# Kernel tuning notes

Hardware: AMD Instinct MI355X
Metric: run time of the kernel (lower is better)

Reference implementation:

```python
import jax, jax.numpy as jnp
import numpy as np
import math

HIDDEN_DIM = 256
H2 = HIDDEN_DIM // 2  # 128
FEATURE_TEMPERATURE = math.sqrt(float(HIDDEN_DIM))


def setup_inputs() -> dict:
    key = jax.random.key(0)
    kf, ks, kw1, kb1, kw2, kb2 = jax.random.split(key, 6)
    B, N, D = 2, 1024, 256
    functional_hidden = jax.random.normal(kf, (B, N, D), dtype=jnp.float32)
    structural_hidden = jax.random.normal(ks, (B, N, D), dtype=jnp.float32)
    # relation_mlp params: Linear(1, H2) then Linear(H2, 1)
    bound1 = 1.0  # fan_in = 1
    w1 = jax.random.uniform(kw1, (H2,), jnp.float32, -bound1, bound1)
    b1 = jax.random.uniform(kb1, (H2,), jnp.float32, -bound1, bound1)
    bound2 = 1.0 / math.sqrt(H2)
    w2 = jax.random.uniform(kw2, (H2,), jnp.float32, -bound2, bound2)
    b2 = jax.random.uniform(kb2, (1,), jnp.float32, -bound2, bound2)
    return {"functional_hidden": functional_hidden, "structural_hidden": structural_hidden,
            "w1": w1, "b1": b1, "w2": w2, "b2": b2}


def reference(functional_hidden, structural_hidden, w1, b1, w2, b2):
    # center along feature dim
    fc = functional_hidden - jnp.mean(functional_hidden, axis=-1, keepdims=True)   # [B,N,D]
    sc = structural_hidden - jnp.mean(structural_hidden, axis=-1, keepdims=True)   # [B,N,D]
    # covariance: [B,N,N]
    covariance = jnp.einsum('bnd,bmd->bnm', fc, sc) / FEATURE_TEMPERATURE
    # per-row std norms (un-normalized, as in source: sqrt of sum of squares)
    f_std = jnp.maximum(jnp.sqrt(jnp.sum(fc * fc, axis=-1)), 1e-6)  # [B,N]
    s_std = jnp.maximum(jnp.sqrt(jnp.sum(sc * sc, axis=-1)), 1e-6)  # [B,N]
    denominator = jnp.maximum(f_std[:, :, None] * s_std[:, None, :], 1e-6)  # [B,N,N]
    correlation = jnp.clip(covariance / denominator, -1.0, 1.0)
    assortativity = jnp.exp(correlation)  # [B,N,N]
    # broadcast 2-layer MLP over every pair: Linear(1,H2)-GELU(exact)-Linear(H2,1)
    h = jax.nn.gelu(assortativity[..., None] * w1 + b1, approximate=False)  # [B,N,N,H2]
    out = jnp.einsum('bnmh,h->bnm', h, w2) + b2[0]  # [B,N,N]
    return out
```

## Files before the change

### kernel.cpp

```cpp
#include <hip/hip_runtime.h>
#include <math.h>

#define NB   2
#define NSEQ 1024
#define DD   256
#define LUTN 2048

#define BM 128
#define BN 64
#define MAGIC 0x5CA1AB1Eu

typedef _Float16 f16;
typedef _Float16 f16x8 __attribute__((ext_vector_type(8)));
typedef float f32x4 __attribute__((ext_vector_type(4)));

__device__ __forceinline__ float wrsum(float v) {
#pragma unroll
  for (int off = 32; off > 0; off >>= 1) v += __shfl_xor(v, off, 64);
  return v;
}

__global__ __launch_bounds__(512, 2) void fused_kernel(
    const float* __restrict__ fg, const float* __restrict__ sg,
    const float* __restrict__ w1, const float* __restrict__ b1,
    const float* __restrict__ w2, const float* __restrict__ b2,
    float* __restrict__ lut, unsigned* __restrict__ flags,
    float* __restrict__ out) {
  __shared__ __align__(16) f16 As[2][BM * 64];
  __shared__ __align__(16) f16 Bs[2][BN * 64];
  __shared__ float lut_s[LUTN + 1];
  __shared__ float mA[BM], rA[BM], mB[BN], rB[BN];

  const int t = threadIdx.x;
  const int lane = t & 63;
  const int w = t >> 6;
  const int wr = w >> 1, wc = w & 1;
  const int la = lane & 15;
  const int kg = lane >> 4;

  const int bid = blockIdx.x;
  const int x = bid & 7, k = bid >> 3;
  const int panel = x + 8 * (k >> 4);
  const int bz  = panel >> 3;
  const int bm0 = (panel & 7) * BM;
  const int bn0 = (k & 15) * BN;

  const float* fb = fg + ((size_t)bz * NSEQ + bm0) * DD;
  const float* sb = sg + ((size_t)bz * NSEQ + bn0) * DD;

  const int sr = t >> 2;
  const int so = t & 3;
  const bool doB = (t < 256);

  float4 A0[2], B0[2], A1[2], B1[2];
  float sAa = 0.f, qAa = 0.f, sBa = 0.f, qBa = 0.f;

  auto ld = [&](float4 (&a)[2], float4 (&b)[2], int st) {
    const float* p = &fb[(size_t)sr * DD + st * 32 + so * 8];
    a[0] = *reinterpret_cast<const float4*>(p);
    a[1] = *reinterpret_cast<const float4*>(p + 4);
    if (doB) {
      const float* q = &sb[(size_t)sr * DD + st * 32 + so * 8];
      b[0] = *reinterpret_cast<const float4*>(q);
      b[1] = *reinterpret_cast<const float4*>(q + 4);
    }
  };

  auto split8 = [](const float4& u0, const float4& u1, f16x8& hv, f16x8& lv,
                   float& sm, float& sq) {
    const float vals[8] = {u0.x, u0.y, u0.z, u0.w, u1.x, u1.y, u1.z, u1.w};
#pragma unroll
    for (int e = 0; e < 8; ++e) {
      sm += vals[e];
      sq = fmaf(vals[e], vals[e], sq);
      const f16 h = (f16)vals[e];
      hv[e] = h;
      lv[e] = (f16)(vals[e] - (float)h);
    }
  };

  auto cvt_write = [&](float4 (&a)[2], float4 (&b)[2], int pbuf) {
    f16x8 hv, lv;
    split8(a[0], a[1], hv, lv, sAa, qAa);
    *reinterpret_cast<f16x8*>(&As[pbuf][sr * 64 + ((so ^ (sr & 7)) << 3)]) = hv;
    *reinterpret_cast<f16x8*>(&As[pbuf][sr * 64 + (((4 + so) ^ (sr & 7)) << 3)]) = lv;
    if (doB) {
      split8(b[0], b[1], hv, lv, sBa, qBa);
      *reinterpret_cast<f16x8*>(&Bs[pbuf][sr * 64 + ((so ^ (sr & 7)) << 3)]) = hv;
      *reinterpret_cast<f16x8*>(&Bs[pbuf][sr * 64 + (((4 + so) ^ (sr & 7)) << 3)]) = lv;
    }
  };

  f32x4 acc[2][2] = {};

  auto do_mfma = [&](int p) {
    f16x8 ah[2], al[2], bh[2], bl[2];
#pragma unroll
    for (int i = 0; i < 2; ++i) {
      const int r = wr * 32 + 16 * i + la;
      ah[i] = *reinterpret_cast<const f16x8*>(&As[p][r * 64 + ((kg ^ (r & 7)) << 3)]);
      al[i] = *reinterpret_cast<const f16x8*>(&As[p][r * 64 + (((4 + kg) ^ (r & 7)) << 3)]);
    }
#pragma unroll
    for (int j = 0; j < 2; ++j) {
      const int r = wc * 32 + 16 * j + la;
      bh[j] = *reinterpret_cast<const f16x8*>(&Bs[p][r * 64 + ((kg ^ (r & 7)) << 3)]);
      bl[j] = *reinterpret_cast<const f16x8*>(&Bs[p][r * 64 + (((4 + kg) ^ (r & 7)) << 3)]);
    }
#pragma unroll
    for (int i = 0; i < 2; ++i)
#pragma unroll
      for (int j = 0; j < 2; ++j) {
        acc[i][j] = __builtin_amdgcn_mfma_f32_16x16x32_f16(ah[i], bh[j], acc[i][j], 0, 0, 0);
        acc[i][j] = __builtin_amdgcn_mfma_f32_16x16x32_f16(ah[i], bl[j], acc[i][j], 0, 0, 0);
        acc[i][j] = __builtin_amdgcn_mfma_f32_16x16x32_f16(al[i], bh[j], acc[i][j], 0, 0, 0);
      }
  };

  ld(A0, B0, 0);

  {
    const float w1a = w1[lane], b1a = b1[lane], w2a = w2[lane];
    const float w1b = w1[lane + 64], b1b = b1[lane + 64], w2b = w2[lane + 64];
    const float b2v = b2[0];
    int e = bid * 8 + w;
#pragma unroll
    for (int pass = 0; pass < 2; ++pass) {
      if (pass == 1) { if (bid == 0 && w == 0) e = LUTN; else break; }
      const float corr = -1.0f + (float)e * (2.0f / LUTN);
      const float a = expf(corr);
      const float x0 = fmaf(a, w1a, b1a);
      const float x1 = fmaf(a, w1b, b1b);
      const float g0 = 0.5f * x0 * (1.0f + erff(x0 * 0.70710678118654752f));
      const float g1 = 0.5f * x1 * (1.0f + erff(x1 * 0.70710678118654752f));
      float acc2 = fmaf(g1, w2b, g0 * w2a);
      acc2 = wrsum(acc2);
      if (lane == 0)
        __hip_atomic_store(&lut[e], acc2 + b2v, __ATOMIC_RELAXED, __HIP_MEMORY_SCOPE_AGENT);
    }
  }

  cvt_write(A0, B0, 0);
  asm volatile("s_waitcnt vmcnt(0)" ::: "memory");
  __syncthreads();
  if (t == 0)
    __hip_atomic_store(&flags[bid], MAGIC, __ATOMIC_RELAXED, __HIP_MEMORY_SCOPE_AGENT);

  ld(A0, B0, 1);
  ld(A1, B1, 2);

#pragma unroll
  for (int st = 0; st < 8; ++st) {
    do_mfma(st & 1);
    if (st < 7) {
      if (st & 1) {
        cvt_write(A1, B1, (st + 1) & 1);
        if (st < 6) ld(A1, B1, st + 3);
      } else {
        cvt_write(A0, B0, (st + 1) & 1);
        if (st < 6) ld(A0, B0, st + 3);
      }
      asm volatile("s_waitcnt lgkmcnt(0)" ::: "memory");
      __builtin_amdgcn_s_barrier();
    }
  }

  auto red4 = [](float v) {
    v += __shfl_xor(v, 1, 64);
    v += __shfl_xor(v, 2, 64);
    return v;
  };
  sAa = red4(sAa); qAa = red4(qAa);
  if ((t & 3) == 0) {
    const float m = sAa * (1.0f / DD);
    mA[sr] = m;
    rA[sr] = 1.0f / fmaxf(sqrtf(fmaxf(qAa - (float)DD * m * m, 0.0f)), 1e-6f);
  }
  if (doB) {
    sBa = red4(sBa); qBa = red4(qBa);
    if ((t & 3) == 0) {
      const float m = sBa * (1.0f / DD);
      mB[sr] = m;
      rB[sr] = 1.0f / fmaxf(sqrtf(fmaxf(qBa - (float)DD * m * m, 0.0f)), 1e-6f);
    }
  }

  if (t < 256)
    while (__hip_atomic_load(&flags[t], __ATOMIC_RELAXED, __HIP_MEMORY_SCOPE_AGENT) != MAGIC) {}
  __syncthreads();
  for (int i = t; i <= LUTN; i += 512)
    lut_s[i] = __hip_atomic_load(&lut[i], __ATOMIC_RELAXED, __HIP_MEMORY_SCOPE_AGENT);
  __syncthreads();

  float msv[2], rsv[2];
#pragma unroll
  for (int j = 0; j < 2; ++j) {
    const int cl = wc * 32 + 16 * j + la;
    msv[j] = mB[cl];
    rsv[j] = rB[cl];
  }
#pragma unroll
  for (int i = 0; i < 2; ++i) {
#pragma unroll
    for (int rg = 0; rg < 4; ++rg) {
      const int rowl = wr * 32 + 16 * i + 4 * kg + rg;
      const float mfv = mA[rowl];
      const float rfv = rA[rowl];
#pragma unroll
      for (int j = 0; j < 2; ++j) {
        const float cov = acc[i][j][rg] * (1.0f / 16.0f) - 16.0f * mfv * msv[j];
        float corr = fminf(fmaxf(cov * rfv * rsv[j], -1.0f), 1.0f);
        const float tf = (corr + 1.0f) * (float)(LUTN / 2);
        int idx = (int)tf;
        idx = idx > (LUTN - 1) ? (LUTN - 1) : idx;
        const float fr = tf - (float)idx;
        const float lo = lut_s[idx], hi = lut_s[idx + 1];
        out[((size_t)bz * NSEQ + bm0 + rowl) * NSEQ + bn0 + wc * 32 + 16 * j + la]
            = fmaf(fr, hi - lo, lo);
      }
    }
  }
}

extern "C" void kernel_launch(void* const* d_in, const int* in_sizes, int n_in,
                              void* d_out, int out_size, void* d_ws, size_t ws_size,
                              hipStream_t stream) {
  const float* f  = (const float*)d_in[0];
  const float* s  = (const float*)d_in[1];
  const float* w1 = (const float*)d_in[2];
  const float* b1 = (const float*)d_in[3];
  const float* w2 = (const float*)d_in[4];
  const float* b2 = (const float*)d_in[5];
  float* out = (float*)d_out;

  char* ws = (char*)d_ws;
  float* lut = (float*)(ws);
  unsigned* flags = (unsigned*)(ws + 16384);

  fused_kernel<<<256, 512, 0, stream>>>(f, s, w1, b1, w2, b2, lut, flags, out);
}
```

Measured before the change: 15.61 us.

## Double K-step depth to 64, rebalance B loads, overlap LUT fetch with last MFMA

Each pipeline stage now covers 64 K-elements split into two LDS sub-buffers, halving the number of barriers from 7 to 3. The B-tile loads are spread across all 512 threads instead of only half. The flag spin-wait and LUT copy into shared memory move inside the final stage so they overlap the last MFMA step, and one barrier is dropped. LDS use doubles, so launch bounds fall to one block per SM, which may reduce occupancy and latency hiding.

Measured after the change: 14.91 us. -4.5%, faster.

```diff
diff --git a/kernel.cpp b/kernel.cpp
--- a/kernel.cpp
+++ b/kernel.cpp
@@ -20,14 +20,14 @@
   return v;
 }
 
-__global__ __launch_bounds__(512, 2) void fused_kernel(
+__global__ __launch_bounds__(512, 1) void fused_kernel(
     const float* __restrict__ fg, const float* __restrict__ sg,
     const float* __restrict__ w1, const float* __restrict__ b1,
     const float* __restrict__ w2, const float* __restrict__ b2,
     float* __restrict__ lut, unsigned* __restrict__ flags,
     float* __restrict__ out) {
-  __shared__ __align__(16) f16 As[2][BM * 64];
-  __shared__ __align__(16) f16 Bs[2][BN * 64];
+  __shared__ __align__(16) f16 As[2][2][BM * 64];
+  __shared__ __align__(16) f16 Bs[2][2][BN * 64];
   __shared__ float lut_s[LUTN + 1];
   __shared__ float mA[BM], rA[BM], mB[BN], rB[BN];
 
@@ -48,22 +48,21 @@
   const float* fb = fg + ((size_t)bz * NSEQ + bm0) * DD;
   const float* sb = sg + ((size_t)bz * NSEQ + bn0) * DD;
 
-  const int sr = t >> 2;
-  const int so = t & 3;
-  const bool doB = (t < 256);
-
-  float4 A0[2], B0[2], A1[2], B1[2];
+  const int ar = t >> 2, ao = t & 3;
+  const int br = t >> 3, bc = (t >> 2) & 1, bo = t & 3;
+
+  float4 A0[4], B0[2], A1[4], B1[2];
   float sAa = 0.f, qAa = 0.f, sBa = 0.f, qBa = 0.f;
 
-  auto ld = [&](float4 (&a)[2], float4 (&b)[2], int st) {
-    const float* p = &fb[(size_t)sr * DD + st * 32 + so * 8];
+  auto ld = [&](float4 (&a)[4], float4 (&b)[2], int st) {
+    const float* p = &fb[(size_t)ar * DD + st * 64 + ao * 8];
     a[0] = *reinterpret_cast<const float4*>(p);
     a[1] = *reinterpret_cast<const float4*>(p + 4);
-    if (doB) {
-      const float* q = &sb[(size_t)sr * DD + st * 32 + so * 8];
-      b[0] = *reinterpret_cast<const float4*>(q);
-      b[1] = *reinterpret_cast<const float4*>(q + 4);
-    }
+    a[2] = *reinterpret_cast<const float4*>(p + 32);
+    a[3] = *reinterpret_cast<const float4*>(p + 36);
+    const float* q = &sb[(size_t)br * DD + st * 64 + bc * 32 + bo * 8];
+    b[0] = *reinterpret_cast<const float4*>(q);
+    b[1] = *reinterpret_cast<const float4*>(q + 4);
   };
 
   auto split8 = [](const float4& u0, const float4& u1, f16x8& hv, f16x8& lv,
@@ -79,42 +78,53 @@
     }
   };
 
-  auto cvt_write = [&](float4 (&a)[2], float4 (&b)[2], int pbuf) {
-    f16x8 hv, lv;
-    split8(a[0], a[1], hv, lv, sAa, qAa);
-    *reinterpret_cast<f16x8*>(&As[pbuf][sr * 64 + ((so ^ (sr & 7)) << 3)]) = hv;
-    *reinterpret_cast<f16x8*>(&As[pbuf][sr * 64 + (((4 + so) ^ (sr & 7)) << 3)]) = lv;
-    if (doB) {
+  auto cvt_write = [&](float4 (&a)[4], float4 (&b)[2], int pbuf) {
+#pragma unroll
+    for (int ch = 0; ch < 2; ++ch) {
+      f16x8 hv, lv;
+      split8(a[2 * ch], a[2 * ch + 1], hv, lv, sAa, qAa);
+      f16* base = &As[pbuf][ch][ar * 64];
+      *reinterpret_cast<f16x8*>(&base[(ao ^ (ar & 7)) << 3]) = hv;
+      *reinterpret_cast<f16x8*>(&base[((4 + ao) ^ (ar & 7)) << 3]) = lv;
+    }
+    {
+      f16x8 hv, lv;
       split8(b[0], b[1], hv, lv, sBa, qBa);
-      *reinterpret_cast<f16x8*>(&Bs[pbuf][sr * 64 + ((so ^ (sr & 7)) << 3)]) = hv;
-      *reinterpret_cast<f16x8*>(&Bs[pbuf][sr * 64 + (((4 + so) ^ (sr & 7)) << 3)]) = lv;
+      f16* base = &Bs[pbuf][bc][br * 64];
+      *reinterpret_cast<f16x8*>(&base[(bo ^ (br & 7)) << 3]) = hv;
+      *reinterpret_cast<f16x8*>(&base[((4 + bo) ^ (br & 7)) << 3]) = lv;
     }
   };
 
   f32x4 acc[2][2] = {};
 
   auto do_mfma = [&](int p) {
-    f16x8 ah[2], al[2], bh[2], bl[2];
-#pragma unroll
-    for (int i = 0; i < 2; ++i) {
-      const int r = wr * 32 + 16 * i + la;
-      ah[i] = *reinterpret_cast<const f16x8*>(&As[p][r * 64 + ((kg ^ (r & 7)) << 3)]);
-      al[i] = *reinterpret_cast<const f16x8*>(&As[p][r * 64 + (((4 + kg) ^ (r & 7)) << 3)]);
-    }
-#pragma unroll
-    for (int j = 0; j < 2; ++j) {
-      const int r = wc * 32 + 16 * j + la;
-      bh[j] = *reinterpret_cast<const f16x8*>(&Bs[p][r * 64 + ((kg ^ (r & 7)) << 3)]);
-      bl[j] = *reinterpret_cast<const f16x8*>(&Bs[p][r * 64 + (((4 + kg) ^ (r & 7)) << 3)]);
-    }
-#pragma unroll
-    for (int i = 0; i < 2; ++i)
+#pragma unroll
+    for (int ks = 0; ks < 2; ++ks) {
+      f16x8 ah[2], al[2], bh[2], bl[2];
+#pragma unroll
+      for (int i = 0; i < 2; ++i) {
+        const int r = wr * 32 + 16 * i + la;
+        const f16* base = &As[p][ks][r * 64];
+        ah[i] = *reinterpret_cast<const f16x8*>(&base[(kg ^ (r & 7)) << 3]);
+        al[i] = *reinterpret_cast<const f16x8*>(&base[((4 + kg) ^ (r & 7)) << 3]);
+      }
 #pragma unroll
       for (int j = 0; j < 2; ++j) {
-        acc[i][j] = __builtin_amdgcn_mfma_f32_16x16x32_f16(ah[i], bh[j], acc[i][j], 0, 0, 0);
-        acc[i][j] = __builtin_amdgcn_mfma_f32_16x16x32_f16(ah[i], bl[j], acc[i][j], 0, 0, 0);
-        acc[i][j] = __builtin_amdgcn_mfma_f32_16x16x32_f16(al[i], bh[j], acc[i][j], 0, 0, 0);
+        const int r = wc * 32 + 16 * j + la;
+        const f16* base = &Bs[p][ks][r * 64];
+        bh[j] = *reinterpret_cast<const f16x8*>(&base[(kg ^ (r & 7)) << 3]);
+        bl[j] = *reinterpret_cast<const f16x8*>(&base[((4 + kg) ^ (r & 7)) << 3]);
       }
+#pragma unroll
+      for (int i = 0; i < 2; ++i)
+#pragma unroll
+        for (int j = 0; j < 2; ++j) {
+          acc[i][j] = __builtin_amdgcn_mfma_f32_16x16x32_f16(ah[i], bh[j], acc[i][j], 0, 0, 0);
+          acc[i][j] = __builtin_amdgcn_mfma_f32_16x16x32_f16(ah[i], bl[j], acc[i][j], 0, 0, 0);
+          acc[i][j] = __builtin_amdgcn_mfma_f32_16x16x32_f16(al[i], bh[j], acc[i][j], 0, 0, 0);
+        }
+    }
   };
 
   ld(A0, B0, 0);
@@ -149,21 +159,25 @@
   ld(A0, B0, 1);
   ld(A1, B1, 2);
 
-#pragma unroll
-  for (int st = 0; st < 8; ++st) {
-    do_mfma(st & 1);
-    if (st < 7) {
-      if (st & 1) {
-        cvt_write(A1, B1, (st + 1) & 1);
-        if (st < 6) ld(A1, B1, st + 3);
-      } else {
-        cvt_write(A0, B0, (st + 1) & 1);
-        if (st < 6) ld(A0, B0, st + 3);
-      }
-      asm volatile("s_waitcnt lgkmcnt(0)" ::: "memory");
-      __builtin_amdgcn_s_barrier();
-    }
-  }
+  do_mfma(0);
+  cvt_write(A0, B0, 1);
+  ld(A0, B0, 3);
+  asm volatile("s_waitcnt lgkmcnt(0)" ::: "memory");
+  __builtin_amdgcn_s_barrier();
+  do_mfma(1);
+  cvt_write(A1, B1, 0);
+  asm volatile("s_waitcnt lgkmcnt(0)" ::: "memory");
+  __builtin_amdgcn_s_barrier();
+  do_mfma(0);
+  cvt_write(A0, B0, 1);
+  if (t < 256)
+    while (__hip_atomic_load(&flags[t], __ATOMIC_RELAXED, __HIP_MEMORY_SCOPE_AGENT) != MAGIC) {}
+#pragma unroll
+  for (int i = t; i <= LUTN; i += 512)
+    lut_s[i] = __hip_atomic_load(&lut[i], __ATOMIC_RELAXED, __HIP_MEMORY_SCOPE_AGENT);
+  asm volatile("s_waitcnt lgkmcnt(0)" ::: "memory");
+  __builtin_amdgcn_s_barrier();
+  do_mfma(1);
 
   auto red4 = [](float v) {
     v += __shfl_xor(v, 1, 64);
@@ -173,23 +187,16 @@
   sAa = red4(sAa); qAa = red4(qAa);
   if ((t & 3) == 0) {
     const float m = sAa * (1.0f / DD);
-    mA[sr] = m;
-    rA[sr] = 1.0f / fmaxf(sqrtf(fmaxf(qAa - (float)DD * m * m, 0.0f)), 1e-6f);
-  }
-  if (doB) {
-    sBa = red4(sBa); qBa = red4(qBa);
-    if ((t & 3) == 0) {
-      const float m = sBa * (1.0f / DD);
-      mB[sr] = m;
-      rB[sr] = 1.0f / fmaxf(sqrtf(fmaxf(qBa - (float)DD * m * m, 0.0f)), 1e-6f);
-    }
-  }
-
-  if (t < 256)
-    while (__hip_atomic_load(&flags[t], __ATOMIC_RELAXED, __HIP_MEMORY_SCOPE_AGENT) != MAGIC) {}
-  __syncthreads();
-  for (int i = t; i <= LUTN; i += 512)
-    lut_s[i] = __hip_atomic_load(&lut[i], __ATOMIC_RELAXED, __HIP_MEMORY_SCOPE_AGENT);
+    mA[ar] = m;
+    rA[ar] = 1.0f / fmaxf(sqrtf(fmaxf(qAa - (float)DD * m * m, 0.0f)), 1e-6f);
+  }
+  sBa = red4(sBa); sBa += __shfl_xor(sBa, 4, 64);
+  qBa = red4(qBa); qBa += __shfl_xor(qBa, 4, 64);
+  if ((t & 7) == 0) {
+    const float m = sBa * (1.0f / DD);
+    mB[br] = m;
+    rB[br] = 1.0f / fmaxf(sqrtf(fmaxf(qBa - (float)DD * m * m, 0.0f)), 1e-6f);
+  }
   __syncthreads();
 
   float msv[2], rsv[2];
```
